# Optimization experiments

Measured on AMD Instinct MI355X. Metric: run time of the kernel, lower is better.

## Reference

```python
import jax, jax.numpy as jnp
import numpy as np

N_NODES = 100000
N_EDGES = 3200000
IN_CH = 128
HID = 128
N_CLASSES = 32
N_GRAPHS = 256


def gcn_conv(x, W, b, src, dst, n_nodes):
    """PyG GCNConv: add self-loops, symmetric deg^-1/2 normalization,
    linear transform, gather-scatter aggregation, bias."""
    xw = x @ W  # [N, out]
    loop = jnp.arange(n_nodes, dtype=src.dtype)
    s = jnp.concatenate([src, loop])  # sources incl. self-loops
    d = jnp.concatenate([dst, loop])  # targets incl. self-loops
    deg = jax.ops.segment_sum(jnp.ones_like(d, dtype=xw.dtype), d,
                              num_segments=n_nodes)
    dinv = jnp.where(deg > 0, jax.lax.rsqrt(deg), 0.0)
    norm = dinv[s] * dinv[d]  # [E+N]
    msgs = xw[s] * norm[:, None]  # gather + scale
    out = jax.ops.segment_sum(msgs, d, num_segments=n_nodes)  # scatter-add
    return out + b


def global_mean_pool(x, batch, n_graphs):
    sums = jax.ops.segment_sum(x, batch, num_segments=n_graphs)
    cnt = jax.ops.segment_sum(jnp.ones((x.shape[0],), x.dtype), batch,
                              num_segments=n_graphs)
    return sums / jnp.maximum(cnt, 1.0)[:, None]


def setup_inputs() -> dict:
    key = jax.random.key(0)
    ks = jax.random.split(key, 9)
    x = jax.random.normal(ks[0], (N_NODES, IN_CH), dtype=jnp.float32)
    edge_index = jax.random.randint(ks[1], (2, N_EDGES), 0, N_NODES, dtype=jnp.int32)
    batch = jnp.sort(jax.random.randint(ks[2], (N_NODES,), 0, N_GRAPHS, dtype=jnp.int32))
    s1 = 1.0 / np.sqrt(IN_CH)
    s2 = 1.0 / np.sqrt(HID)
    W1 = jax.random.uniform(ks[3], (IN_CH, HID), jnp.float32, -s1, s1)
    b1 = jnp.zeros((HID,), jnp.float32)
    W2 = jax.random.uniform(ks[4], (HID, HID), jnp.float32, -s2, s2)
    b2 = jnp.zeros((HID,), jnp.float32)
    Wfc = jax.random.uniform(ks[5], (HID, N_CLASSES), jnp.float32, -s2, s2)
    bfc = jax.random.uniform(ks[6], (N_CLASSES,), jnp.float32, -s2, s2)
    return {"x": x, "edge_index": edge_index, "batch": batch,
            "W1": W1, "b1": b1, "W2": W2, "b2": b2, "Wfc": Wfc, "bfc": bfc}


def reference(x, edge_index, batch, W1, b1, W2, b2, Wfc, bfc):
    src, dst = edge_index[0], edge_index[1]
    h = jax.nn.relu(gcn_conv(x, W1, b1, src, dst, N_NODES))
    h = jax.nn.relu(gcn_conv(h, W2, b2, src, dst, N_NODES))
    g = global_mean_pool(h, batch, N_GRAPHS)  # [G, HID]
    return g @ Wfc + bfc  # [G, N_CLASSES]
```

## Files before the change

kernel.cpp:

```cpp
#include <hip/hip_runtime.h>
#include <hip/hip_bf16.h>
#include <hip/hip_fp16.h>

static constexpr int CH     = 128;
static constexpr int NCLS   = 32;
static constexpr int NGRAPH = 256;

static constexpr int BSHIFT = 9;
static constexpr int BW     = 1 << BSHIFT;
static constexpr int MAXB   = 256;

typedef _Float16 half8 __attribute__((ext_vector_type(8)));
typedef _Float16 half4 __attribute__((ext_vector_type(4)));
typedef float    f32x4 __attribute__((ext_vector_type(4)));
typedef float    f32x2 __attribute__((ext_vector_type(2)));

static constexpr float FP8_SCALE = 64.0f;
static constexpr float FP8_INV   = 1.0f / 64.0f;

__device__ __forceinline__ f32x2 dec8(unsigned short u) {
  return __builtin_amdgcn_cvt_pk_f32_fp8((int)u, false);
}
__device__ __forceinline__ unsigned char enc8(float v) {
  return (unsigned char)(__builtin_amdgcn_cvt_pk_fp8_f32(v, v, 0, false) & 0xFF);
}

__global__ __launch_bounds__(256) void k_init_wt(
    int* __restrict__ gcur, int CAP, int NBUCK,
    const float* __restrict__ W1, const float* __restrict__ W2,
    _Float16* __restrict__ WhT1, _Float16* __restrict__ WhT2) {
  int t = threadIdx.x;
  if (blockIdx.x == 0) {
    if (t < NBUCK) gcur[t] = t * CAP;
    return;
  }
  int i = (blockIdx.x - 1) * 256 + t;
  const float* W = (i < CH * CH) ? W1 : W2;
  _Float16* T   = (i < CH * CH) ? WhT1 : WhT2;
  int j = i & (CH * CH - 1);
  int k = j >> 7, n = j & 127;
  T[n * CH + k] = (_Float16)W[j];
}

__global__ __launch_bounds__(1024) void k_scatter(
    const int* __restrict__ src, const int* __restrict__ dst,
    int* __restrict__ gcur, int* __restrict__ ebuf, int E) {
  __shared__ int bcnt[MAXB];
  __shared__ int bbase[MAXB];
  int t = threadIdx.x;
  if (t < MAXB) bcnt[t] = 0;
  __syncthreads();
  int base = blockIdx.x * 8192;
  int s_[8], d_[8], r_[8];
  #pragma unroll
  for (int j = 0; j < 8; ++j) {
    int i = base + j * 1024 + t;
    if (i < E) {
      s_[j] = src[i];
      d_[j] = dst[i];
      r_[j] = atomicAdd(&bcnt[d_[j] >> BSHIFT], 1);
    }
  }
  __syncthreads();
  if (t < MAXB && bcnt[t]) bbase[t] = atomicAdd(&gcur[t], bcnt[t]);
  __syncthreads();
  #pragma unroll
  for (int j = 0; j < 8; ++j) {
    int i = base + j * 1024 + t;
    if (i < E) {
      int b = d_[j] >> BSHIFT;
      int p = ((d_[j] & (BW - 1)) << 17) | s_[j];
      ebuf[bbase[b] + r_[j]] = p;
    }
  }
}

__global__ __launch_bounds__(1024) void k_build(
    const int* __restrict__ ebuf, const int* __restrict__ gcur,
    int* __restrict__ offs, int* __restrict__ oend,
    float* __restrict__ dinv, int* __restrict__ csr, int N, int CAP) {
  __shared__ int sdeg[BW];
  __shared__ int sscan[BW];
  int b = blockIdx.x;
  int t = threadIdx.x;
  int lo = b << BSHIFT;
  int e0 = b * CAP;
  int e1 = gcur[b];

  if (t < BW) sdeg[t] = 0;
  __syncthreads();
  for (int e = e0 + t; e < e1; e += 1024)
    atomicAdd(&sdeg[ebuf[e] >> 17], 1);
  __syncthreads();
  if (t < BW) sscan[t] = sdeg[t];
  __syncthreads();
  for (int st = 1; st < BW; st <<= 1) {
    int v = (t < BW && t >= st) ? sscan[t - st] : 0;
    __syncthreads();
    if (t < BW) sscan[t] += v;
    __syncthreads();
  }
  if (t < BW) {
    int ex = b * CAP + sscan[t] - sdeg[t];
    int n = lo + t;
    if (n < N) {
      offs[n] = ex;
      oend[n] = ex + sdeg[t];
      dinv[n] = 1.0f / sqrtf((float)(sdeg[t] + 1));
    }
    sscan[t] = ex;
  }
  __syncthreads();
  for (int e = e0 + t; e < e1; e += 1024) {
    int p = ebuf[e];
    int pos = atomicAdd(&sscan[p >> 17], 1);
    csr[pos] = p & 0x1FFFF;
  }
}

__device__ __forceinline__ void stage_w(const _Float16* __restrict__ WhT,
                                        _Float16 (*Ws)[136], int tid) {
  #pragma unroll
  for (int l = 0; l < 8; ++l) {
    int idx = tid + l * 256;
    int n = idx >> 4, k8 = (idx & 15) << 3;
    *(half8*)&Ws[n][k8] = *(const half8*)(WhT + n * CH + k8);
  }
}

__device__ __forceinline__ void gemm_core64(
    const _Float16 (*As)[136], const _Float16 (*Ws)[136],
    const float* __restrict__ dinv, unsigned char* __restrict__ C,
    int row0, int M, int tid) {
  int lane = tid & 63, wave = tid >> 6;
  int quad = lane >> 4, sub = lane & 15;
  int m0 = wave * 16;

  f32x4 acc[8];
  #pragma unroll
  for (int j = 0; j < 8; ++j) acc[j] = (f32x4){0.f, 0.f, 0.f, 0.f};

  #pragma unroll
  for (int kc = 0; kc < 4; ++kc) {
    int ko = kc * 32 + quad * 8;
    half8 a = *(const half8*)&As[m0 + sub][ko];
    #pragma unroll
    for (int nt = 0; nt < 8; ++nt) {
      half8 b = *(const half8*)&Ws[nt * 16 + sub][ko];
      acc[nt] = __builtin_amdgcn_mfma_f32_16x16x32_f16(a, b, acc[nt], 0, 0, 0);
    }
  }
  #pragma unroll
  for (int r = 0; r < 4; ++r) {
    int row = row0 + m0 + quad * 4 + r;
    if (row < M) {
      float d = dinv[row] * FP8_SCALE;
      #pragma unroll
      for (int nt = 0; nt < 8; ++nt)
        C[(size_t)row * CH + nt * 16 + sub] = enc8(acc[nt][r] * d);
    }
  }
}

__global__ __launch_bounds__(256) void k_gemm_f32(
    const float* __restrict__ A, const _Float16* __restrict__ WhT,
    const float* __restrict__ dinv, unsigned char* __restrict__ C, int M) {
  __shared__ _Float16 As[64][136];
  __shared__ _Float16 Ws[128][136];
  int tid = threadIdx.x;
  int row0 = blockIdx.x * 64;
  #pragma unroll
  for (int l = 0; l < 8; ++l) {
    int idx = tid + l * 256;
    int r = idx >> 5, c4 = (idx & 31) << 2;
    int rr = row0 + r; if (rr >= M) rr = M - 1;
    float4 v = *(const float4*)(A + (size_t)rr * CH + c4);
    half4 hv = { (_Float16)v.x, (_Float16)v.y, (_Float16)v.z, (_Float16)v.w };
    *(half4*)&As[r][c4] = hv;
  }
  stage_w(WhT, Ws, tid);
  __syncthreads();
  gemm_core64(As, Ws, dinv, C, row0, M, tid);
}

__global__ __launch_bounds__(256) void k_gemm_f16(
    const _Float16* __restrict__ A, const _Float16* __restrict__ WhT,
    const float* __restrict__ dinv, unsigned char* __restrict__ C, int M) {
  __shared__ _Float16 As[64][136];
  __shared__ _Float16 Ws[128][136];
  int tid = threadIdx.x;
  int row0 = blockIdx.x * 64;
  #pragma unroll
  for (int l = 0; l < 4; ++l) {
    int idx = tid + l * 256;
    int r = idx >> 4, c8 = (idx & 15) << 3;
    int rr = row0 + r; if (rr >= M) rr = M - 1;
    *(half8*)&As[r][c8] = *(const half8*)(A + (size_t)rr * CH + c8);
  }
  stage_w(WhT, Ws, tid);
  __syncthreads();
  gemm_core64(As, Ws, dinv, C, row0, M, tid);
}

__global__ __launch_bounds__(256) void k_agg(
    const unsigned char* __restrict__ xs, const int* __restrict__ csr,
    const int* __restrict__ offs, const int* __restrict__ oend,
    const float* __restrict__ dinv, const float* __restrict__ bias,
    __half* __restrict__ out, int N) {
  int wid  = blockIdx.x * 4 + (threadIdx.x >> 6);
  int lane = threadIdx.x & 63;
  int nA = wid * 2, nB = nA + 1;
  if (nA >= N) return;
  bool hasB = (nB < N);
  const unsigned short* base = (const unsigned short*)xs;

  int eA = offs[nA], endA = oend[nA];
  int eB = hasB ? offs[nB] : 0;
  int endB = hasB ? oend[nB] : 0;

  f32x2 sfA = dec8(base[(size_t)nA * 64 + lane]);
  float axA = sfA[0], ayA = sfA[1], bxA = 0.f, byA = 0.f;
  float axB = 0.f, ayB = 0.f, bxB = 0.f, byB = 0.f;
  if (hasB) {
    f32x2 sfB = dec8(base[(size_t)nB * 64 + lane]);
    axB = sfB[0]; ayB = sfB[1];
  }

  while (eA + 4 <= endA && eB + 4 <= endB) {
    int a0 = csr[eA], a1 = csr[eA + 1], a2 = csr[eA + 2], a3 = csr[eA + 3];
    int b0 = csr[eB], b1 = csr[eB + 1], b2 = csr[eB + 2], b3 = csr[eB + 3];
    unsigned short uA0 = base[(size_t)a0 * 64 + lane];
    unsigned short uA1 = base[(size_t)a1 * 64 + lane];
    unsigned short uA2 = base[(size_t)a2 * 64 + lane];
    unsigned short uA3 = base[(size_t)a3 * 64 + lane];
    unsigned short uB0 = base[(size_t)b0 * 64 + lane];
    unsigned short uB1 = base[(size_t)b1 * 64 + lane];
    unsigned short uB2 = base[(size_t)b2 * 64 + lane];
    unsigned short uB3 = base[(size_t)b3 * 64 + lane];
    f32x2 vA0 = dec8(uA0), vA1 = dec8(uA1), vA2 = dec8(uA2), vA3 = dec8(uA3);
    f32x2 vB0 = dec8(uB0), vB1 = dec8(uB1), vB2 = dec8(uB2), vB3 = dec8(uB3);
    axA += vA0[0] + vA2[0]; ayA += vA0[1] + vA2[1];
    bxA += vA1[0] + vA3[0]; byA += vA1[1] + vA3[1];
    axB += vB0[0] + vB2[0]; ayB += vB0[1] + vB2[1];
    bxB += vB1[0] + vB3[0]; byB += vB1[1] + vB3[1];
    eA += 4; eB += 4;
  }

  auto tail = [&](int e, int end, float& ax, float& ay, float& bx, float& by) {
    if (e >= end) return;
    int endm1 = end - 1;
    for (; e < end; e += 4) {
      int p1 = e + 1 < endm1 ? e + 1 : endm1;
      int p2 = e + 2 < endm1 ? e + 2 : endm1;
      int p3 = e + 3 < endm1 ? e + 3 : endm1;
      int s0 = csr[e], s1 = csr[p1], s2 = csr[p2], s3 = csr[p3];
      unsigned short u0 = base[(size_t)s0 * 64 + lane];
      unsigned short u1 = base[(size_t)s1 * 64 + lane];
      unsigned short u2 = base[(size_t)s2 * 64 + lane];
      unsigned short u3 = base[(size_t)s3 * 64 + lane];
      f32x2 v0 = dec8(u0), v1 = dec8(u1), v2 = dec8(u2), v3 = dec8(u3);
      float m1 = (e + 1 < end) ? 1.f : 0.f;
      float m2 = (e + 2 < end) ? 1.f : 0.f;
      float m3 = (e + 3 < end) ? 1.f : 0.f;
      ax += v0[0];                 ay += v0[1];
      bx  = fmaf(v1[0], m1, bx);   by  = fmaf(v1[1], m1, by);
      ax  = fmaf(v2[0], m2, ax);   ay  = fmaf(v2[1], m2, ay);
      bx  = fmaf(v3[0], m3, bx);   by  = fmaf(v3[1], m3, by);
    }
  };
  tail(eA, endA, axA, ayA, bxA, byA);
  if (hasB) tail(eB, endB, axB, ayB, bxB, byB);

  float bx0 = bias[2 * lane], bx1 = bias[2 * lane + 1];
  {
    float dn = dinv[nA] * FP8_INV;
    float rx = fmaf(axA + bxA, dn, bx0);
    float ry = fmaf(ayA + byA, dn, bx1);
    ((__half2*)out)[(size_t)nA * 64 + lane] =
        __floats2half2_rn(fmaxf(rx, 0.f), fmaxf(ry, 0.f));
  }
  if (hasB) {
    float dn = dinv[nB] * FP8_INV;
    float rx = fmaf(axB + bxB, dn, bx0);
    float ry = fmaf(ayB + byB, dn, bx1);
    ((__half2*)out)[(size_t)nB * 64 + lane] =
        __floats2half2_rn(fmaxf(rx, 0.f), fmaxf(ry, 0.f));
  }
}

__global__ __launch_bounds__(128) void k_pool(
    const __half* __restrict__ h, const int* __restrict__ batch,
    float* __restrict__ gsum, int* __restrict__ gstart,
    int* __restrict__ gend, int N) {
  int ch = threadIdx.x;
  int n0 = blockIdx.x * 128;
  int n1 = n0 + 128; if (n1 > N) n1 = N;
  if (n0 >= N) return;
  for (int n = n0 + ch; n < n1; n += 128) {
    int g = batch[n];
    if (n == 0 || batch[n - 1] != g) gstart[g] = n;
    if (n == N - 1 || batch[n + 1] != g) gend[g] = n + 1;
  }
  float acc = 0.f;
  int curg = batch[n0];
  for (int n = n0; n < n1; ++n) {
    int g = batch[n];
    if (g != curg) {
      atomicAdd(&gsum[curg * CH + ch], acc);
      acc = 0.f; curg = g;
    }
    acc += __half2float(h[(size_t)n * CH + ch]);
  }
  atomicAdd(&gsum[curg * CH + ch], acc);
}

__global__ __launch_bounds__(64) void k_fc(
    const float* __restrict__ gsum, const int* __restrict__ gstart,
    const int* __restrict__ gend, const float* __restrict__ Wfc,
    const float* __restrict__ bfc, float* __restrict__ outp) {
  int g = blockIdx.x;
  int j = threadIdx.x;
  if (j >= NCLS) return;
  int cnt = gend[g] - gstart[g];
  float invc = 1.0f / fmaxf((float)cnt, 1.0f);
  float acc = 0.0f;
  for (int c = 0; c < CH; ++c)
    acc = fmaf(gsum[g * CH + c], Wfc[c * NCLS + j], acc);
  outp[g * NCLS + j] = fmaf(acc, invc, bfc[j]);
}

extern "C" void kernel_launch(void* const* d_in, const int* in_sizes, int n_in,
                              void* d_out, int out_size, void* d_ws, size_t ws_size,
                              hipStream_t stream) {
  const float* x    = (const float*)d_in[0];
  const int*   ei   = (const int*)d_in[1];
  const int*   batch= (const int*)d_in[2];
  const float* W1   = (const float*)d_in[3];
  const float* b1   = (const float*)d_in[4];
  const float* W2   = (const float*)d_in[5];
  const float* b2   = (const float*)d_in[6];
  const float* Wfc  = (const float*)d_in[7];
  const float* bfc  = (const float*)d_in[8];
  float* outp = (float*)d_out;

  const int N = in_sizes[0] / CH;
  const int E = in_sizes[1] / 2;
  const int* src = ei;
  const int* dst = ei + E;
  const int NBUCK = (N + BW - 1) >> BSHIFT;
  const int CAP = (E / NBUCK) + (E / NBUCK) / 8 + 256;

  char* w = (char*)d_ws;
  size_t o = 0;
  auto carve = [&](size_t bytes) -> void* {
    o = (o + 255) & ~(size_t)255;
    void* p = w + o;
    o += bytes;
    return p;
  };
  float*    gsum   = (float*)   carve((size_t)NGRAPH * CH * 4);
  int*      gstart = (int*)     carve((size_t)NGRAPH * 4);
  int*      gend   = (int*)     carve((size_t)NGRAPH * 4);
  size_t zbytes = o;
  int*      offs   = (int*)     carve((size_t)N * 4);
  int*      oendb  = (int*)     carve((size_t)N * 4);
  int*      gcur   = (int*)     carve(MAXB * 4);
  int*      csr    = (int*)     carve((size_t)NBUCK * CAP * 4);
  float*    dinv   = (float*)   carve((size_t)N * 4);
  _Float16* WhT1   = (_Float16*)carve((size_t)CH * CH * 2);
  _Float16* WhT2   = (_Float16*)carve((size_t)CH * CH * 2);
  unsigned char* xsbuf = (unsigned char*)carve((size_t)N * CH);
  __half*   hbuf   = (__half*)  carve((size_t)N * CH * 2);
  (void)ws_size;

  int* ebuf = (int*)hbuf;

  (void)hipMemsetAsync(gsum, 0, zbytes, stream);

  const int GB64 = (N + 63) / 64;
  const int GB   = (N + 127) / 128;
  const int AB   = (N + 7) / 8;

  k_init_wt<<<129, 256, 0, stream>>>(gcur, CAP, NBUCK, W1, W2, WhT1, WhT2);
  k_scatter<<<(E + 8191) / 8192, 1024, 0, stream>>>(src, dst, gcur, ebuf, E);
  k_build  <<<NBUCK, 1024, 0, stream>>>(ebuf, gcur, offs, oendb, dinv, csr, N, CAP);

  k_gemm_f32<<<GB64, 256, 0, stream>>>(x, WhT1, dinv, xsbuf, N);
  k_agg<<<AB, 256, 0, stream>>>(xsbuf, csr, offs, oendb, dinv, b1, hbuf, N);
  k_gemm_f16<<<GB64, 256, 0, stream>>>((const _Float16*)hbuf, WhT2, dinv, xsbuf, N);
  k_agg<<<AB, 256, 0, stream>>>(xsbuf, csr, offs, oendb, dinv, b2, hbuf, N);

  k_pool<<<GB, 128, 0, stream>>>(hbuf, batch, gsum, gstart, gend, N);
  k_fc<<<NGRAPH, 64, 0, stream>>>(gsum, gstart, gend, Wfc, bfc, outp);
  (void)out_size; (void)n_in;
}
```

Measured before the change: 368.1 us.

## Pad CSR rows to multiples of four with a zero dummy node for vector index loads

Pads each node's CSR neighbour list to a multiple of four, filling the padding with a dummy node index N whose fp8 feature row is zeroed. The aggregation kernel can then load indices as int4 and drop the masked tail logic, and it uses 32-bit address arithmetic. The bucket width is halved (more buckets, MAXB raised) and the per-bucket capacity is enlarged to absorb the padding. The cost is extra padded gathers hitting the dummy row, plus more scatter and build blocks.

```diff
diff --git a/kernel.cpp b/kernel.cpp
--- a/kernel.cpp
+++ b/kernel.cpp
@@ -6,9 +6,9 @@
 static constexpr int NCLS   = 32;
 static constexpr int NGRAPH = 256;
 
-static constexpr int BSHIFT = 9;
+static constexpr int BSHIFT = 8;
 static constexpr int BW     = 1 << BSHIFT;
-static constexpr int MAXB   = 256;
+static constexpr int MAXB   = 512;
 
 typedef _Float16 half8 __attribute__((ext_vector_type(8)));
 typedef _Float16 half4 __attribute__((ext_vector_type(4)));
@@ -26,12 +26,13 @@
 }
 
 __global__ __launch_bounds__(256) void k_init_wt(
-    int* __restrict__ gcur, int CAP, int NBUCK,
+    int* __restrict__ gcur, int CAP, int NBUCK, int* __restrict__ xzero,
     const float* __restrict__ W1, const float* __restrict__ W2,
     _Float16* __restrict__ WhT1, _Float16* __restrict__ WhT2) {
   int t = threadIdx.x;
   if (blockIdx.x == 0) {
-    if (t < NBUCK) gcur[t] = t * CAP;
+    for (int i = t; i < NBUCK; i += 256) gcur[i] = i * CAP;
+    if (t < 32) xzero[t] = 0;
     return;
   }
   int i = (blockIdx.x - 1) * 256 + t;
@@ -92,7 +93,7 @@
   for (int e = e0 + t; e < e1; e += 1024)
     atomicAdd(&sdeg[ebuf[e] >> 17], 1);
   __syncthreads();
-  if (t < BW) sscan[t] = sdeg[t];
+  if (t < BW) sscan[t] = (sdeg[t] + 3) & ~3;
   __syncthreads();
   for (int st = 1; st < BW; st <<= 1) {
     int v = (t < BW && t >= st) ? sscan[t - st] : 0;
@@ -101,12 +102,15 @@
     __syncthreads();
   }
   if (t < BW) {
-    int ex = b * CAP + sscan[t] - sdeg[t];
+    int deg  = sdeg[t];
+    int pdeg = (deg + 3) & ~3;
+    int ex = b * CAP + sscan[t] - pdeg;
     int n = lo + t;
     if (n < N) {
       offs[n] = ex;
-      oend[n] = ex + sdeg[t];
-      dinv[n] = 1.0f / sqrtf((float)(sdeg[t] + 1));
+      oend[n] = ex + deg;
+      dinv[n] = 1.0f / sqrtf((float)(deg + 1));
+      for (int q = deg; q < pdeg; ++q) csr[ex + q] = N;
     }
     sscan[t] = ex;
   }
@@ -212,77 +216,67 @@
   int nA = wid * 2, nB = nA + 1;
   if (nA >= N) return;
   bool hasB = (nB < N);
-  const unsigned short* base = (const unsigned short*)xs;
-
-  int eA = offs[nA], endA = oend[nA];
+  unsigned int lane2 = (unsigned int)lane << 1;
+
+  int eA = offs[nA];
+  int cA = (oend[nA] - eA + 3) >> 2;
   int eB = hasB ? offs[nB] : 0;
-  int endB = hasB ? oend[nB] : 0;
-
-  f32x2 sfA = dec8(base[(size_t)nA * 64 + lane]);
-  float axA = sfA[0], ayA = sfA[1], bxA = 0.f, byA = 0.f;
-  float axB = 0.f, ayB = 0.f, bxB = 0.f, byB = 0.f;
-  if (hasB) {
-    f32x2 sfB = dec8(base[(size_t)nB * 64 + lane]);
-    axB = sfB[0]; ayB = sfB[1];
-  }
-
-  while (eA + 4 <= endA && eB + 4 <= endB) {
-    int a0 = csr[eA], a1 = csr[eA + 1], a2 = csr[eA + 2], a3 = csr[eA + 3];
-    int b0 = csr[eB], b1 = csr[eB + 1], b2 = csr[eB + 2], b3 = csr[eB + 3];
-    unsigned short uA0 = base[(size_t)a0 * 64 + lane];
-    unsigned short uA1 = base[(size_t)a1 * 64 + lane];
-    unsigned short uA2 = base[(size_t)a2 * 64 + lane];
-    unsigned short uA3 = base[(size_t)a3 * 64 + lane];
-    unsigned short uB0 = base[(size_t)b0 * 64 + lane];
-    unsigned short uB1 = base[(size_t)b1 * 64 + lane];
-    unsigned short uB2 = base[(size_t)b2 * 64 + lane];
-    unsigned short uB3 = base[(size_t)b3 * 64 + lane];
-    f32x2 vA0 = dec8(uA0), vA1 = dec8(uA1), vA2 = dec8(uA2), vA3 = dec8(uA3);
-    f32x2 vB0 = dec8(uB0), vB1 = dec8(uB1), vB2 = dec8(uB2), vB3 = dec8(uB3);
-    axA += vA0[0] + vA2[0]; ayA += vA0[1] + vA2[1];
-    bxA += vA1[0] + vA3[0]; byA += vA1[1] + vA3[1];
-    axB += vB0[0] + vB2[0]; ayB += vB0[1] + vB2[1];
-    bxB += vB1[0] + vB3[0]; byB += vB1[1] + vB3[1];
-    eA += 4; eB += 4;
-  }
-
-  auto tail = [&](int e, int end, float& ax, float& ay, float& bx, float& by) {
-    if (e >= end) return;
-    int endm1 = end - 1;
-    for (; e < end; e += 4) {
-      int p1 = e + 1 < endm1 ? e + 1 : endm1;
-      int p2 = e + 2 < endm1 ? e + 2 : endm1;
-      int p3 = e + 3 < endm1 ? e + 3 : endm1;
-      int s0 = csr[e], s1 = csr[p1], s2 = csr[p2], s3 = csr[p3];
-      unsigned short u0 = base[(size_t)s0 * 64 + lane];
-      unsigned short u1 = base[(size_t)s1 * 64 + lane];
-      unsigned short u2 = base[(size_t)s2 * 64 + lane];
-      unsigned short u3 = base[(size_t)s3 * 64 + lane];
-      f32x2 v0 = dec8(u0), v1 = dec8(u1), v2 = dec8(u2), v3 = dec8(u3);
-      float m1 = (e + 1 < end) ? 1.f : 0.f;
-      float m2 = (e + 2 < end) ? 1.f : 0.f;
-      float m3 = (e + 3 < end) ? 1.f : 0.f;
-      ax += v0[0];                 ay += v0[1];
-      bx  = fmaf(v1[0], m1, bx);   by  = fmaf(v1[1], m1, by);
-      ax  = fmaf(v2[0], m2, ax);   ay  = fmaf(v2[1], m2, ay);
-      bx  = fmaf(v3[0], m3, bx);   by  = fmaf(v3[1], m3, by);
-    }
-  };
-  tail(eA, endA, axA, ayA, bxA, byA);
-  if (hasB) tail(eB, endB, axB, ayB, bxB, byB);
-
-  float bx0 = bias[2 * lane], bx1 = bias[2 * lane + 1];
+  int cB = hasB ? ((oend[nB] - eB + 3) >> 2) : 0;
+
+  f32x2 aA0 = dec8(*(const unsigned short*)(xs + (((unsigned int)nA << 7) | lane2)));
+  f32x2 aA1 = {0.f, 0.f};
+  f32x2 aB0 = {0.f, 0.f}, aB1 = {0.f, 0.f};
+  if (hasB)
+    aB0 = dec8(*(const unsigned short*)(xs + (((unsigned int)nB << 7) | lane2)));
+
+  while (cA > 0 && cB > 0) {
+    int4 ca = *(const int4*)(csr + eA);
+    int4 cb = *(const int4*)(csr + eB);
+    unsigned short uA0 = *(const unsigned short*)(xs + (((unsigned int)ca.x << 7) | lane2));
+    unsigned short uA1 = *(const unsigned short*)(xs + (((unsigned int)ca.y << 7) | lane2));
+    unsigned short uA2 = *(const unsigned short*)(xs + (((unsigned int)ca.z << 7) | lane2));
+    unsigned short uA3 = *(const unsigned short*)(xs + (((unsigned int)ca.w << 7) | lane2));
+    unsigned short uB0 = *(const unsigned short*)(xs + (((unsigned int)cb.x << 7) | lane2));
+    unsigned short uB1 = *(const unsigned short*)(xs + (((unsigned int)cb.y << 7) | lane2));
+    unsigned short uB2 = *(const unsigned short*)(xs + (((unsigned int)cb.z << 7) | lane2));
+    unsigned short uB3 = *(const unsigned short*)(xs + (((unsigned int)cb.w << 7) | lane2));
+    aA0 += dec8(uA0); aA1 += dec8(uA1); aA0 += dec8(uA2); aA1 += dec8(uA3);
+    aB0 += dec8(uB0); aB1 += dec8(uB1); aB0 += dec8(uB2); aB1 += dec8(uB3);
+    eA += 4; eB += 4; --cA; --cB;
+  }
+  while (cA > 0) {
+    int4 ca = *(const int4*)(csr + eA);
+    unsigned short u0 = *(const unsigned short*)(xs + (((unsigned int)ca.x << 7) | lane2));
+    unsigned short u1 = *(const unsigned short*)(xs + (((unsigned int)ca.y << 7) | lane2));
+    unsigned short u2 = *(const unsigned short*)(xs + (((unsigned int)ca.z << 7) | lane2));
+    unsigned short u3 = *(const unsigned short*)(xs + (((unsigned int)ca.w << 7) | lane2));
+    aA0 += dec8(u0); aA1 += dec8(u1); aA0 += dec8(u2); aA1 += dec8(u3);
+    eA += 4; --cA;
+  }
+  while (cB > 0) {
+    int4 cb = *(const int4*)(csr + eB);
+    unsigned short u0 = *(const unsigned short*)(xs + (((unsigned int)cb.x << 7) | lane2));
+    unsigned short u1 = *(const unsigned short*)(xs + (((unsigned int)cb.y << 7) | lane2));
+    unsigned short u2 = *(const unsigned short*)(xs + (((unsigned int)cb.z << 7) | lane2));
+    unsigned short u3 = *(const unsigned short*)(xs + (((unsigned int)cb.w << 7) | lane2));
+    aB0 += dec8(u0); aB1 += dec8(u1); aB0 += dec8(u2); aB1 += dec8(u3);
+    eB += 4; --cB;
+  }
+
+  float2 bxy = *(const float2*)(bias + 2 * lane);
   {
+    f32x2 s = aA0 + aA1;
     float dn = dinv[nA] * FP8_INV;
-    float rx = fmaf(axA + bxA, dn, bx0);
-    float ry = fmaf(ayA + byA, dn, bx1);
+    float rx = fmaf(s[0], dn, bxy.x);
+    float ry = fmaf(s[1], dn, bxy.y);
     ((__half2*)out)[(size_t)nA * 64 + lane] =
         __floats2half2_rn(fmaxf(rx, 0.f), fmaxf(ry, 0.f));
   }
   if (hasB) {
+    f32x2 s = aB0 + aB1;
     float dn = dinv[nB] * FP8_INV;
-    float rx = fmaf(axB + bxB, dn, bx0);
-    float ry = fmaf(ayB + byB, dn, bx1);
+    float rx = fmaf(s[0], dn, bxy.x);
+    float ry = fmaf(s[1], dn, bxy.y);
     ((__half2*)out)[(size_t)nB * 64 + lane] =
         __floats2half2_rn(fmaxf(rx, 0.f), fmaxf(ry, 0.f));
   }
@@ -348,7 +342,8 @@
   const int* src = ei;
   const int* dst = ei + E;
   const int NBUCK = (N + BW - 1) >> BSHIFT;
-  const int CAP = (E / NBUCK) + (E / NBUCK) / 8 + 256;
+  int CAP = (E / NBUCK) + (E / NBUCK) / 8 + 1280;
+  CAP = (CAP + 3) & ~3;
 
   char* w = (char*)d_ws;
   size_t o = 0;
@@ -369,7 +364,7 @@
   float*    dinv   = (float*)   carve((size_t)N * 4);
   _Float16* WhT1   = (_Float16*)carve((size_t)CH * CH * 2);
   _Float16* WhT2   = (_Float16*)carve((size_t)CH * CH * 2);
-  unsigned char* xsbuf = (unsigned char*)carve((size_t)N * CH);
+  unsigned char* xsbuf = (unsigned char*)carve((size_t)(N + 1) * CH);
   __half*   hbuf   = (__half*)  carve((size_t)N * CH * 2);
   (void)ws_size;
 
@@ -381,7 +376,9 @@
   const int GB   = (N + 127) / 128;
   const int AB   = (N + 7) / 8;
 
-  k_init_wt<<<129, 256, 0, stream>>>(gcur, CAP, NBUCK, W1, W2, WhT1, WhT2);
+  k_init_wt<<<129, 256, 0, stream>>>(gcur, CAP, NBUCK,
+                                     (int*)(xsbuf + (size_t)N * CH),
+                                     W1, W2, WhT1, WhT2);
   k_scatter<<<(E + 8191) / 8192, 1024, 0, stream>>>(src, dst, gcur, ebuf, E);
   k_build  <<<NBUCK, 1024, 0, stream>>>(ebuf, gcur, offs, oendb, dinv, csr, N, CAP);
 
```

Result: faster. 360.5 us (-2.1%).
